# Kernel tuning notes

Hardware: AMD Instinct MI355X
Metric: run time of the kernel (lower is better)

Reference implementation:

```python
import jax, jax.numpy as jnp
import numpy as np

B, H, S, DK = 2, 16, 2048, 64


def setup_inputs() -> dict:
    key = jax.random.key(0)
    kq, kk, kv = jax.random.split(key, 3)
    query = jax.random.normal(kq, (B, H, S, DK), dtype=jnp.float32)
    k = jax.random.normal(kk, (B, H, S, DK), dtype=jnp.float32)
    value = jax.random.normal(kv, (B, H, S, DK), dtype=jnp.float32)
    # causal padding-style mask: 1 = keep, 0 = masked (set to -inf pre-softmax)
    mask = jnp.tril(jnp.ones((S, S), dtype=jnp.int32))[None, None, :, :]
    return {"query": query, "key": k, "value": value, "d_k": DK, "mask": mask}


def reference(query, key, value, d_k, mask):
    # scores: [B, H, Sq, Sk]
    scores = jnp.einsum("bhqd,bhkd->bhqk", query, key)
    scores = scores / jnp.sqrt(jnp.asarray(d_k, dtype=scores.dtype))
    scores = jnp.where(mask == 0, -jnp.inf, scores)
    att = jax.nn.softmax(scores, axis=-1)
    # dropout is identity in eval mode (deterministic reference)
    out = jnp.einsum("bhqk,bhkd->bhqd", att, value)
    return out
```

## Files before the change

kernel.cpp:

```cpp
#include <hip/hip_runtime.h>
#include <cstdint>

#define B_ 2
#define H_ 16
#define S_ 2048
#define DK_ 64
#define BH_ (B_*H_)
#define NQT 32

typedef __attribute__((ext_vector_type(8))) short short8;
typedef __attribute__((ext_vector_type(4))) short short4v;
typedef __attribute__((ext_vector_type(4))) float floatx4;

__device__ inline unsigned short f2bf(float f) {
  union { float f; unsigned u; } v; v.f = f;
  unsigned u = v.u;
  unsigned r = u + 0x7fffu + ((u >> 16) & 1u);
  return (unsigned short)(r >> 16);
}

__device__ inline floatx4 mfma16(short4v a, short4v b, floatx4 c) {
#if __has_builtin(__builtin_amdgcn_mfma_f32_16x16x16bf16_1k)
  return __builtin_amdgcn_mfma_f32_16x16x16bf16_1k(a, b, c, 0, 0, 0);
#else
  asm("v_mfma_f32_16x16x16_bf16 %0, %1, %2, %0" : "+v"(c) : "v"(a), "v"(b));
  return c;
#endif
}

__device__ inline short4v u2s4(unsigned a, unsigned b) {
  union { unsigned u[2]; short4v s; } v;
  v.u[0] = a; v.u[1] = b;
  return v.s;
}

__global__ __launch_bounds__(256) void conv_kv(const float* __restrict__ K,
                                               const float* __restrict__ V,
                                               unsigned short* __restrict__ Kb,
                                               unsigned short* __restrict__ Vb) {
  __shared__ __align__(16) unsigned short t[64 * 80];
  const int bh = blockIdx.y, s0 = blockIdx.x * 64;
  const int row = threadIdx.x >> 2, cp = threadIdx.x & 3;

  {
    const float* src = K + ((size_t)(bh * S_ + s0 + row)) * DK_ + cp * 16;
    unsigned short* dst = Kb + ((size_t)(bh * S_ + s0 + row)) * DK_ + cp * 16;
    #pragma unroll
    for (int h = 0; h < 2; ++h) {
      float4 a = *(const float4*)(src + h * 8);
      float4 b = *(const float4*)(src + h * 8 + 4);
      uint4 st;
      st.x = (unsigned)f2bf(a.x) | ((unsigned)f2bf(a.y) << 16);
      st.y = (unsigned)f2bf(a.z) | ((unsigned)f2bf(a.w) << 16);
      st.z = (unsigned)f2bf(b.x) | ((unsigned)f2bf(b.y) << 16);
      st.w = (unsigned)f2bf(b.z) | ((unsigned)f2bf(b.w) << 16);
      *(uint4*)(dst + h * 8) = st;
    }
  }
  {
    const float* src = V + ((size_t)(bh * S_ + s0 + row)) * DK_ + cp * 16;
    #pragma unroll
    for (int j4 = 0; j4 < 4; ++j4) {
      float4 a = *(const float4*)(src + j4 * 4);
      int c = cp * 16 + j4 * 4;
      t[(c + 0) * 80 + row] = f2bf(a.x);
      t[(c + 1) * 80 + row] = f2bf(a.y);
      t[(c + 2) * 80 + row] = f2bf(a.z);
      t[(c + 3) * 80 + row] = f2bf(a.w);
    }
    __syncthreads();
    const int base128 = s0 & ~127;
    const int t2 = 2 * ((s0 >> 6) & 1) + (cp >> 1);
    const int h  = cp & 1;
    unsigned short* dst = Vb + ((size_t)(bh * DK_ + row)) * S_ + base128 + t2 * 32 + h * 4;
    #pragma unroll
    for (int q = 0; q < 4; ++q)
      *(uint2*)(dst + q * 8) = *(const uint2*)&t[row * 80 + cp * 16 + q * 4];
  }
}

__global__ __launch_bounds__(256, 4)
void fa_kernel(const float* __restrict__ Q, const unsigned short* __restrict__ Kb,
               const unsigned short* __restrict__ Vb, float* __restrict__ Out) {
  __shared__ __align__(16) unsigned short Kt[2][4096];
  __shared__ __align__(16) unsigned short Vt[2][4096];

  const int tid  = threadIdx.x;
  const int wave = tid >> 6;
  const int lane = tid & 63;
  const int quad = lane >> 4;
  const int l16  = lane & 15;
  const int wq   = wave;

  const int id = blockIdx.x;
  const int bh = (id & 7) | (((id >> 3) & 3) << 3);
  const int qt = id >> 5;
  const int nkv = qt + 1;

  const float SCL = 0.125f * 1.44269504088896340736f;

  short8 qf[2];
  {
    const float* p = Q + ((size_t)bh * S_ + qt * 64 + wq * 16 + l16) * DK_ + quad * 8;
    #pragma unroll
    for (int ks = 0; ks < 2; ++ks) {
      float4 x = *(const float4*)(p + ks * 32);
      float4 y = *(const float4*)(p + ks * 32 + 4);
      short8 t;
      t[0]=(short)f2bf(x.x*SCL); t[1]=(short)f2bf(x.y*SCL); t[2]=(short)f2bf(x.z*SCL); t[3]=(short)f2bf(x.w*SCL);
      t[4]=(short)f2bf(y.x*SCL); t[5]=(short)f2bf(y.y*SCL); t[6]=(short)f2bf(y.z*SCL); t[7]=(short)f2bf(y.w*SCL);
      qf[ks] = t;
    }
  }

  floatx4 Ot[4];
  float ls = 0.f;
  #pragma unroll
  for (int d = 0; d < 4; ++d) Ot[d] = (floatx4){0,0,0,0};

  auto stage = [&](int buf, int kv) {
    #pragma unroll
    for (int rd = 0; rd < 2; ++rd) {
      const int cid = rd * 256 + wave * 64 + lane;
      const int row = cid >> 3;
      const int c   = (cid & 7) ^ (row & 7);
      {
        const unsigned short* g = Kb + (((size_t)bh * S_ + kv * 64 + row) << 6) + (c << 3);
        __builtin_amdgcn_global_load_lds(
            (const __attribute__((address_space(1))) void*)g,
            (__attribute__((address_space(3))) void*)&Kt[buf][(rd * 4 + wave) * 512], 16, 0, 0);
      }
      {
        const unsigned short* g = Vb + (((size_t)bh * DK_ + row) << 11) + kv * 64 + (c << 3);
        __builtin_amdgcn_global_load_lds(
            (const __attribute__((address_space(1))) void*)g,
            (__attribute__((address_space(3))) void*)&Vt[buf][(rd * 4 + wave) * 512], 16, 0, 0);
      }
    }
  };

  auto computeT = [&](int cur, bool domask) {
    unsigned pk[4][2];
    #pragma unroll
    for (int nt = 0; nt < 4; ++nt) {
      if (domask && nt > wq) continue;
      const int row = nt * 16 + l16;
      floatx4 s0 = (floatx4){0,0,0,0};
      #pragma unroll
      for (int ks = 0; ks < 2; ++ks) {
        const int p = (ks * 4 + quad) ^ (l16 & 7);
        const short8 ak = *(const short8*)&Kt[cur][row * 64 + p * 8];
        s0 = __builtin_amdgcn_mfma_f32_16x16x32_bf16(ak, qf[ks], s0, 0, 0, 0);
      }
      if (domask && nt == wq) {
        #pragma unroll
        for (int r = 0; r < 4; ++r)
          if (quad * 4 + r > l16) s0[r] = -INFINITY;
      }
      float e0 = __builtin_amdgcn_exp2f(s0[0]);
      float e1 = __builtin_amdgcn_exp2f(s0[1]);
      float e2 = __builtin_amdgcn_exp2f(s0[2]);
      float e3 = __builtin_amdgcn_exp2f(s0[3]);
      ls += (e0 + e1) + (e2 + e3);
      pk[nt][0] = __builtin_amdgcn_perm(__float_as_uint(e1) + 0x8000u,
                                        __float_as_uint(e0) + 0x8000u, 0x07060302u);
      pk[nt][1] = __builtin_amdgcn_perm(__float_as_uint(e3) + 0x8000u,
                                        __float_as_uint(e2) + 0x8000u, 0x07060302u);
    }
    __builtin_amdgcn_s_setprio(1);
    #pragma unroll
    for (int dblk = 0; dblk < 4; ++dblk) {
      const int row = dblk * 16 + l16;
      #pragma unroll
      for (int tt = 0; tt < 2; ++tt) {
        if (domask && 2 * tt > wq) continue;
        const int p = (tt * 4 + quad) ^ (l16 & 7);
        const short8 v8 = *(const short8*)&Vt[cur][row * 64 + p * 8];
        const short4v vlo = __builtin_shufflevector(v8, v8, 0, 1, 2, 3);
        const short4v vhi = __builtin_shufflevector(v8, v8, 4, 5, 6, 7);
        Ot[dblk] = mfma16(vlo, u2s4(pk[2*tt  ][0], pk[2*tt  ][1]), Ot[dblk]);
        if (!(domask && 2 * tt + 1 > wq))
          Ot[dblk] = mfma16(vhi, u2s4(pk[2*tt+1][0], pk[2*tt+1][1]), Ot[dblk]);
      }
    }
    __builtin_amdgcn_s_setprio(0);
  };

  stage(0, 0);
  __syncthreads();
  int kv = 0;
  for (; kv < nkv - 1; ++kv) {
    const int cur = kv & 1;
    stage(cur ^ 1, kv + 1);
    computeT(cur, false);
    __syncthreads();
  }
  computeT(kv & 1, true);

  ls += __shfl_xor(ls, 16);
  ls += __shfl_xor(ls, 32);
  const float inv = 1.0f / ls;
  float* og = Out + ((size_t)bh * S_ + qt * 64 + wq * 16 + l16) * DK_;
  #pragma unroll
  for (int dblk = 0; dblk < 4; ++dblk) {
    floatx4 tot = Ot[dblk] * inv;
    *(floatx4*)(og + dblk * 16 + quad * 4) = tot;
  }
}

extern "C" void kernel_launch(void* const* d_in, const int* in_sizes, int n_in,
                              void* d_out, int out_size, void* d_ws, size_t ws_size,
                              hipStream_t stream) {
  const float* Q = (const float*)d_in[0];
  const float* K = (const float*)d_in[1];
  const float* V = (const float*)d_in[2];
  float* Out = (float*)d_out;
  unsigned short* Kb = (unsigned short*)d_ws;
  unsigned short* Vb = Kb + (size_t)BH_ * S_ * DK_;
  conv_kv<<<dim3(S_ / 64, BH_), 256, 0, stream>>>(K, V, Kb, Vb);
  fa_kernel<<<dim3(NQT * BH_), 256, 0, stream>>>(Q, Kb, Vb, Out);
}
```

Measured before the change: 145.8 us.

## Switch attention to 32x32x16 MFMA with split-KV waves and LDS reduction

Replaces the 16x16 MFMA tiles with 32x32x16 bf16 MFMA. Each pair of waves now splits the 64-key tile in half and shares a 32-row query block, and their partial outputs and row sums are combined through LDS at the end. It also uses hardware packed bf16 conversion plus permlane32 swaps to build the P operand, changes the V layout to plain transposed rows, and reorders query tiles across blocks to balance the causal workload. The aim is fewer MFMA issues and better load balance, at the cost of an extra LDS reduction and a wasted wave pair on diagonal tiles.

```diff
diff --git a/kernel.cpp b/kernel.cpp
--- a/kernel.cpp
+++ b/kernel.cpp
@@ -9,8 +9,8 @@
 #define NQT 32
 
 typedef __attribute__((ext_vector_type(8))) short short8;
-typedef __attribute__((ext_vector_type(4))) short short4v;
 typedef __attribute__((ext_vector_type(4))) float floatx4;
+typedef __attribute__((ext_vector_type(16))) float floatx16;
 
 __device__ inline unsigned short f2bf(float f) {
   union { float f; unsigned u; } v; v.f = f;
@@ -19,19 +19,8 @@
   return (unsigned short)(r >> 16);
 }
 
-__device__ inline floatx4 mfma16(short4v a, short4v b, floatx4 c) {
-#if __has_builtin(__builtin_amdgcn_mfma_f32_16x16x16bf16_1k)
-  return __builtin_amdgcn_mfma_f32_16x16x16bf16_1k(a, b, c, 0, 0, 0);
-#else
-  asm("v_mfma_f32_16x16x16_bf16 %0, %1, %2, %0" : "+v"(c) : "v"(a), "v"(b));
-  return c;
-#endif
-}
-
-__device__ inline short4v u2s4(unsigned a, unsigned b) {
-  union { unsigned u[2]; short4v s; } v;
-  v.u[0] = a; v.u[1] = b;
-  return v.s;
+__device__ inline floatx16 mfma32(short8 a, short8 b, floatx16 c) {
+  return __builtin_amdgcn_mfma_f32_32x32x16_bf16(a, b, c, 0, 0, 0);
 }
 
 __global__ __launch_bounds__(256) void conv_kv(const float* __restrict__ K,
@@ -69,142 +58,157 @@
       t[(c + 3) * 80 + row] = f2bf(a.w);
     }
     __syncthreads();
-    const int base128 = s0 & ~127;
-    const int t2 = 2 * ((s0 >> 6) & 1) + (cp >> 1);
-    const int h  = cp & 1;
-    unsigned short* dst = Vb + ((size_t)(bh * DK_ + row)) * S_ + base128 + t2 * 32 + h * 4;
-    #pragma unroll
-    for (int q = 0; q < 4; ++q)
-      *(uint2*)(dst + q * 8) = *(const uint2*)&t[row * 80 + cp * 16 + q * 4];
+    unsigned short* dst = Vb + ((size_t)(bh * DK_ + row)) * S_ + s0 + cp * 16;
+    *(uint4*)(dst + 0) = *(const uint4*)&t[row * 80 + cp * 16];
+    *(uint4*)(dst + 8) = *(const uint4*)&t[row * 80 + cp * 16 + 8];
   }
 }
 
 __global__ __launch_bounds__(256, 4)
 void fa_kernel(const float* __restrict__ Q, const unsigned short* __restrict__ Kb,
                const unsigned short* __restrict__ Vb, float* __restrict__ Out) {
-  __shared__ __align__(16) unsigned short Kt[2][4096];
-  __shared__ __align__(16) unsigned short Vt[2][4096];
+  __shared__ __align__(16) unsigned short SMEM[2 * 8192 + 256];
 
   const int tid  = threadIdx.x;
   const int wave = tid >> 6;
   const int lane = tid & 63;
-  const int quad = lane >> 4;
-  const int l16  = lane & 15;
-  const int wq   = wave;
+  const int l31  = lane & 31;
+  const int h    = lane >> 5;
+  const int wq   = wave >> 1;
+  const int ws   = wave & 1;
 
   const int id = blockIdx.x;
-  const int bh = (id & 7) | (((id >> 3) & 3) << 3);
-  const int qt = id >> 5;
+  const int bh = id & 31;
+  const int u  = id >> 5;
+  const int r  = u & 7, k4 = u >> 3;
+  const int qt = (k4 == 0) ? r : (k4 == 1) ? (15 - r) : (k4 == 2) ? (16 + r) : (31 - r);
   const int nkv = qt + 1;
 
   const float SCL = 0.125f * 1.44269504088896340736f;
 
-  short8 qf[2];
+  short8 qf[4];
   {
-    const float* p = Q + ((size_t)bh * S_ + qt * 64 + wq * 16 + l16) * DK_ + quad * 8;
-    #pragma unroll
-    for (int ks = 0; ks < 2; ++ks) {
-      float4 x = *(const float4*)(p + ks * 32);
-      float4 y = *(const float4*)(p + ks * 32 + 4);
+    const float* qp = Q + ((size_t)bh * S_ + qt * 64 + wq * 32 + l31) * DK_ + h * 8;
+    #pragma unroll
+    for (int dstep = 0; dstep < 4; ++dstep) {
+      float4 x = *(const float4*)(qp + dstep * 16);
+      float4 y = *(const float4*)(qp + dstep * 16 + 4);
       short8 t;
       t[0]=(short)f2bf(x.x*SCL); t[1]=(short)f2bf(x.y*SCL); t[2]=(short)f2bf(x.z*SCL); t[3]=(short)f2bf(x.w*SCL);
       t[4]=(short)f2bf(y.x*SCL); t[5]=(short)f2bf(y.y*SCL); t[6]=(short)f2bf(y.z*SCL); t[7]=(short)f2bf(y.w*SCL);
-      qf[ks] = t;
-    }
-  }
-
-  floatx4 Ot[4];
+      qf[dstep] = t;
+    }
+  }
+
+  floatx16 Ot[2] = { {0,0,0,0,0,0,0,0,0,0,0,0,0,0,0,0},
+                     {0,0,0,0,0,0,0,0,0,0,0,0,0,0,0,0} };
   float ls = 0.f;
-  #pragma unroll
-  for (int d = 0; d < 4; ++d) Ot[d] = (floatx4){0,0,0,0};
-
-  auto stage = [&](int buf, int kv) {
+
+  auto stage = [&](int slot, int kv) {
     #pragma unroll
     for (int rd = 0; rd < 2; ++rd) {
-      const int cid = rd * 256 + wave * 64 + lane;
+      const int cid = rd * 256 + tid;
       const int row = cid >> 3;
       const int c   = (cid & 7) ^ (row & 7);
       {
         const unsigned short* g = Kb + (((size_t)bh * S_ + kv * 64 + row) << 6) + (c << 3);
         __builtin_amdgcn_global_load_lds(
             (const __attribute__((address_space(1))) void*)g,
-            (__attribute__((address_space(3))) void*)&Kt[buf][(rd * 4 + wave) * 512], 16, 0, 0);
+            (__attribute__((address_space(3))) void*)&SMEM[slot * 8192 + rd * 2048 + wave * 512],
+            16, 0, 0);
       }
       {
-        const unsigned short* g = Vb + (((size_t)bh * DK_ + row) << 11) + kv * 64 + (c << 3);
+        const unsigned short* g = Vb + (((size_t)(bh * DK_ + row)) << 11) + kv * 64 + (c << 3);
         __builtin_amdgcn_global_load_lds(
             (const __attribute__((address_space(1))) void*)g,
-            (__attribute__((address_space(3))) void*)&Vt[buf][(rd * 4 + wave) * 512], 16, 0, 0);
+            (__attribute__((address_space(3))) void*)&SMEM[slot * 8192 + 4096 + rd * 2048 + wave * 512],
+            16, 0, 0);
       }
     }
   };
 
-  auto computeT = [&](int cur, bool domask) {
-    unsigned pk[4][2];
-    #pragma unroll
-    for (int nt = 0; nt < 4; ++nt) {
-      if (domask && nt > wq) continue;
-      const int row = nt * 16 + l16;
-      floatx4 s0 = (floatx4){0,0,0,0};
+  auto computeT = [&](int cur, bool diag) {
+    if (diag && wq == 0 && ws == 1) return;
+    const unsigned short* Kt = SMEM + cur * 8192;
+    const unsigned short* Vt = Kt + 4096;
+    floatx16 s = {0,0,0,0,0,0,0,0,0,0,0,0,0,0,0,0};
+    const int krow = ws * 32 + l31;
+    #pragma unroll
+    for (int dstep = 0; dstep < 4; ++dstep) {
+      const short8 a = *(const short8*)&Kt[krow * 64 + (((dstep << 1) + h) ^ (krow & 7)) * 8];
+      s = mfma32(a, qf[dstep], s);
+    }
+    if (diag && wq == ws) {
       #pragma unroll
-      for (int ks = 0; ks < 2; ++ks) {
-        const int p = (ks * 4 + quad) ^ (l16 & 7);
-        const short8 ak = *(const short8*)&Kt[cur][row * 64 + p * 8];
-        s0 = __builtin_amdgcn_mfma_f32_16x16x32_bf16(ak, qf[ks], s0, 0, 0, 0);
-      }
-      if (domask && nt == wq) {
+      for (int rg = 0; rg < 16; ++rg) {
+        const int sl = (rg & 3) + 8 * (rg >> 2) + 4 * h;
+        if (sl > l31) s[rg] = -INFINITY;
+      }
+    }
+    float e[16];
+    #pragma unroll
+    for (int i = 0; i < 16; ++i) e[i] = __builtin_amdgcn_exp2f(s[i]);
+    ls += (((e[0]+e[1])+(e[2]+e[3])) + ((e[4]+e[5])+(e[6]+e[7])))
+        + (((e[8]+e[9])+(e[10]+e[11])) + ((e[12]+e[13])+(e[14]+e[15])));
+    short8 pb[2];
+    #pragma unroll
+    for (int t = 0; t < 2; ++t) {
+      unsigned X0, X1, Y0, Y1;
+      asm("v_cvt_pk_bf16_f32 %0, %1, %2" : "=v"(X0) : "v"(e[8*t+0]), "v"(e[8*t+1]));
+      asm("v_cvt_pk_bf16_f32 %0, %1, %2" : "=v"(X1) : "v"(e[8*t+2]), "v"(e[8*t+3]));
+      asm("v_cvt_pk_bf16_f32 %0, %1, %2" : "=v"(Y0) : "v"(e[8*t+4]), "v"(e[8*t+5]));
+      asm("v_cvt_pk_bf16_f32 %0, %1, %2" : "=v"(Y1) : "v"(e[8*t+6]), "v"(e[8*t+7]));
+      asm("v_permlane32_swap_b32 %0, %1" : "+v"(X0), "+v"(Y0));
+      asm("v_permlane32_swap_b32 %0, %1" : "+v"(X1), "+v"(Y1));
+      union { unsigned u[4]; short8 s8; } pbu;
+      pbu.u[0] = X0; pbu.u[1] = X1; pbu.u[2] = Y0; pbu.u[3] = Y1;
+      pb[t] = pbu.s8;
+    }
+    #pragma unroll
+    for (int dsub = 0; dsub < 2; ++dsub) {
+      const int vrow = dsub * 32 + l31;
+      const short8 v0 = *(const short8*)&Vt[vrow * 64 + (((ws << 2) + h    ) ^ (vrow & 7)) * 8];
+      const short8 v1 = *(const short8*)&Vt[vrow * 64 + (((ws << 2) + h + 2) ^ (vrow & 7)) * 8];
+      Ot[dsub] = mfma32(v0, pb[0], Ot[dsub]);
+      Ot[dsub] = mfma32(v1, pb[1], Ot[dsub]);
+    }
+  };
+
+  stage(0, 0);
+  for (int kv = 0; kv < nkv; ++kv) {
+    asm volatile("s_waitcnt vmcnt(0)" ::: "memory");
+    __builtin_amdgcn_s_barrier();
+    if (kv + 1 < nkv) stage((kv + 1) & 1, kv + 1);
+    computeT(kv & 1, kv == nkv - 1);
+  }
+
+  ls += __shfl_xor(ls, 32);
+  float* OP = (float*)SMEM;
+  float* LP = OP + 4096;
+  __syncthreads();
+  if (ws == 1) {
+    #pragma unroll
+    for (int dsub = 0; dsub < 2; ++dsub)
+      #pragma unroll
+      for (int rg = 0; rg < 16; ++rg)
+        OP[((wq * 2 + dsub) * 16 + rg) * 64 + lane] = Ot[dsub][rg];
+    LP[wq * 64 + lane] = ls;
+  }
+  __syncthreads();
+  if (ws == 0) {
+    const float inv = 1.0f / (ls + LP[wq * 64 + lane]);
+    float* og = Out + ((size_t)(bh * S_ + qt * 64 + wq * 32 + l31)) * DK_;
+    #pragma unroll
+    for (int dsub = 0; dsub < 2; ++dsub) {
+      #pragma unroll
+      for (int g = 0; g < 4; ++g) {
+        floatx4 o;
         #pragma unroll
-        for (int r = 0; r < 4; ++r)
-          if (quad * 4 + r > l16) s0[r] = -INFINITY;
-      }
-      float e0 = __builtin_amdgcn_exp2f(s0[0]);
-      float e1 = __builtin_amdgcn_exp2f(s0[1]);
-      float e2 = __builtin_amdgcn_exp2f(s0[2]);
-      float e3 = __builtin_amdgcn_exp2f(s0[3]);
-      ls += (e0 + e1) + (e2 + e3);
-      pk[nt][0] = __builtin_amdgcn_perm(__float_as_uint(e1) + 0x8000u,
-                                        __float_as_uint(e0) + 0x8000u, 0x07060302u);
-      pk[nt][1] = __builtin_amdgcn_perm(__float_as_uint(e3) + 0x8000u,
-                                        __float_as_uint(e2) + 0x8000u, 0x07060302u);
-    }
-    __builtin_amdgcn_s_setprio(1);
-    #pragma unroll
-    for (int dblk = 0; dblk < 4; ++dblk) {
-      const int row = dblk * 16 + l16;
-      #pragma unroll
-      for (int tt = 0; tt < 2; ++tt) {
-        if (domask && 2 * tt > wq) continue;
-        const int p = (tt * 4 + quad) ^ (l16 & 7);
-        const short8 v8 = *(const short8*)&Vt[cur][row * 64 + p * 8];
-        const short4v vlo = __builtin_shufflevector(v8, v8, 0, 1, 2, 3);
-        const short4v vhi = __builtin_shufflevector(v8, v8, 4, 5, 6, 7);
-        Ot[dblk] = mfma16(vlo, u2s4(pk[2*tt  ][0], pk[2*tt  ][1]), Ot[dblk]);
-        if (!(domask && 2 * tt + 1 > wq))
-          Ot[dblk] = mfma16(vhi, u2s4(pk[2*tt+1][0], pk[2*tt+1][1]), Ot[dblk]);
-      }
-    }
-    __builtin_amdgcn_s_setprio(0);
-  };
-
-  stage(0, 0);
-  __syncthreads();
-  int kv = 0;
-  for (; kv < nkv - 1; ++kv) {
-    const int cur = kv & 1;
-    stage(cur ^ 1, kv + 1);
-    computeT(cur, false);
-    __syncthreads();
-  }
-  computeT(kv & 1, true);
-
-  ls += __shfl_xor(ls, 16);
-  ls += __shfl_xor(ls, 32);
-  const float inv = 1.0f / ls;
-  float* og = Out + ((size_t)bh * S_ + qt * 64 + wq * 16 + l16) * DK_;
-  #pragma unroll
-  for (int dblk = 0; dblk < 4; ++dblk) {
-    floatx4 tot = Ot[dblk] * inv;
-    *(floatx4*)(og + dblk * 16 + quad * 4) = tot;
+        for (int j = 0; j < 4; ++j)
+          o[j] = (Ot[dsub][4 * g + j] + OP[((wq * 2 + dsub) * 16 + 4 * g + j) * 64 + lane]) * inv;
+        *(floatx4*)(og + dsub * 32 + 8 * g + 4 * h) = o;
+      }
+    }
   }
 }
 
```

Measured after the change: 131.9 us (median of 2 runs). 9.6% less time.
